# Optimization experiments

Hardware: AMD Instinct MI355X
Metric: run time of the kernel (lower is better)

The kernel has to match this reference:

```python
import jax, jax.numpy as jnp
import numpy as np


def setup_inputs() -> dict:
    key = jax.random.key(0)
    k1, k2, k3, k4 = jax.random.split(key, 4)
    N, F_in, F_out = 8192, 512, 256
    inp = jax.random.normal(k1, (N, F_in), dtype=jnp.float32)
    adj = jax.random.uniform(k2, (N, N), dtype=jnp.float32)
    stdv = 1.0 / np.sqrt(F_out)
    weight = jax.random.uniform(k3, (F_in, F_out), minval=-stdv, maxval=stdv, dtype=jnp.float32)
    b = jax.random.uniform(k4, (F_out,), minval=-stdv, maxval=stdv, dtype=jnp.float32)
    return {"input": inp, "adj": adj, "weight": weight, "b": b}


def reference(input, adj, weight, b):
    N = adj.shape[0]
    degree = jnp.sum(adj, axis=1)                      # [N]
    # A_tilde = 2*I - adj
    A_tilde = 2.0 * jnp.eye(N, dtype=adj.dtype) - adj
    d_inv_sqrt = 1.0 / jnp.sqrt(2.0 + degree)          # [N]
    # D^-1/2 @ A_tilde @ D^-1/2 as broadcasted row/col scaling (same math, O(N^2))
    L_sharpen = d_inv_sqrt[:, None] * A_tilde * d_inv_sqrt[None, :]
    support = input @ weight                           # [N, F_out]
    out = L_sharpen @ support + b                      # [N, F_out]
    return jax.nn.relu(out)
```

## Files before the change

kernel.cpp:

```cpp
#include <hip/hip_runtime.h>


typedef _Float16 h4 __attribute__((ext_vector_type(4)));
typedef _Float16 h8 __attribute__((ext_vector_type(8)));
typedef float f4 __attribute__((ext_vector_type(4)));

__device__ __forceinline__ void gload_lds16(const void* g, void* l) {
    __builtin_amdgcn_global_load_lds(
        (const __attribute__((address_space(1))) void*)g,
        (__attribute__((address_space(3))) void*)l, 16, 0, 0);
}

__global__ __launch_bounds__(256) void k0_wt(const float* __restrict__ weight,
                                             char* __restrict__ wt) {
    const int idx = blockIdx.x * 256 + threadIdx.x;
    const int k = idx >> 8, j = idx & 255;
    const _Float16 h = (_Float16)weight[idx];
    const int off = j * 1024 + ((k >> 6) << 7) + (((k & 63) << 1) ^ ((j & 7) << 4));
    *(_Float16*)(wt + off) = h;
}

__global__ __launch_bounds__(256) void k1_deg(const float* __restrict__ adj,
                                              float* __restrict__ dinv) {
    const int r = blockIdx.x;
    const float4* rp = (const float4*)(adj + (size_t)r * 8192);
    const int t = threadIdx.x;
    float s = 0.f;
#pragma unroll
    for (int i = 0; i < 8; ++i) {
        float4 v = rp[t + i * 256];
        s += (v.x + v.y) + (v.z + v.w);
    }
#pragma unroll
    for (int off = 32; off > 0; off >>= 1) s += __shfl_down(s, off, 64);
    __shared__ float part[4];
    if ((t & 63) == 0) part[t >> 6] = s;
    __syncthreads();
    if (t == 0) {
        float deg = (part[0] + part[1]) + (part[2] + part[3]);
        dinv[r] = 1.0f / sqrtf(2.0f + deg);
    }
}

__global__ __launch_bounds__(512) void k2_support(const float* __restrict__ input,
                                                  const char* __restrict__ wt,
                                                  const float* __restrict__ dinv,
                                                  char* __restrict__ sT) {
    __shared__ char smem[8192 + 32768];
    const int t = threadIdx.x, w = t >> 6, l = t & 63;
    const int r0 = (int)blockIdx.x * 64;
    const int ar = t >> 4, ac4 = t & 15;
    const int bj = l >> 3, bb = (l & 7) * 16;

    f4 acc[4][2] = {};

    for (int kt = 0; kt < 8; ++kt) {
        const int k0 = kt * 64;
        __syncthreads();
#pragma unroll
        for (int hh = 0; hh < 2; ++hh) {
            const int row = ar + hh * 32;
            float4 v = *(const float4*)(input + (size_t)(r0 + row) * 512 + k0 + ac4 * 4);
            h4 h;
            h[0] = (_Float16)v.x; h[1] = (_Float16)v.y;
            h[2] = (_Float16)v.z; h[3] = (_Float16)v.w;
            *(h4*)(smem + row * 128 + ((ac4 * 8) ^ ((row & 7) << 4))) = h;
        }
#pragma unroll
        for (int q = 0; q < 4; ++q) {
            const int c = w * 4 + q;
            gload_lds16(wt + (size_t)(c * 8 + bj) * 1024 + kt * 128 + bb,
                        smem + 8192 + c * 1024);
        }
        __syncthreads();
#pragma unroll
        for (int kk = 0; kk < 2; ++kk) {
            const int kb = (kk * 32 + ((l >> 4) << 3)) << 1;
            h8 b[2];
#pragma unroll
            for (int n = 0; n < 2; ++n) {
                const int j = w * 32 + n * 16 + (l & 15);
                b[n] = *(const h8*)(smem + 8192 + j * 128 + (kb ^ ((j & 7) << 4)));
            }
#pragma unroll
            for (int m = 0; m < 4; ++m) {
                const int r = m * 16 + (l & 15);
                h8 a = *(const h8*)(smem + r * 128 + (kb ^ ((r & 7) << 4)));
                acc[m][0] = __builtin_amdgcn_mfma_f32_16x16x32_f16(a, b[0], acc[m][0], 0, 0, 0);
                acc[m][1] = __builtin_amdgcn_mfma_f32_16x16x32_f16(a, b[1], acc[m][1], 0, 0, 0);
            }
        }
    }
#pragma unroll
    for (int m = 0; m < 4; ++m)
#pragma unroll
        for (int n = 0; n < 2; ++n) {
            const int j = w * 32 + n * 16 + (l & 15);
            const int k0r = r0 + m * 16 + ((l >> 4) << 2);
            h4 h;
#pragma unroll
            for (int r = 0; r < 4; ++r)
                h[r] = (_Float16)(dinv[k0r + r] * acc[m][n][r]);
            const int off = j * 16384 + ((k0r >> 6) << 7) +
                            (((k0r & 63) << 1) ^ ((j & 7) << 4));
            *(h4*)(sT + off) = h;
        }
}

__global__ __launch_bounds__(512, 4) void k3_spmm(const float* __restrict__ adj,
                                                  const char* __restrict__ sT,
                                                  float* __restrict__ part,
                                                  float* __restrict__ out,
                                                  int steps) {
    __shared__ __align__(16) char smem[2][40960];
    const int t = threadIdx.x;
    const int w = t >> 6, l = t & 63;
    const int wm = w >> 2, wn = w & 3;
    const int i0 = (int)blockIdx.x * 64;
    const int ks0 = (int)blockIdx.y * steps * 64;

    const int arow = t >> 3;
    const int ak8 = (t & 7) * 8;
    const int arow_g = i0 + arow;
    const float4* aptr = (const float4*)(adj + (size_t)arow_g * 8192 + ks0 + ak8);
    const int a_off = arow * 128 + (((t & 7) << 4) ^ ((arow & 7) << 4));

    const int bj = l >> 3, bb = (l & 7) * 16;
    const int chunk0 = ks0 >> 6;

    f4 acc[2][4] = {};

    auto stageB = [&](int kt, int buf) {
        char* bl = smem[buf] + 8192;
#pragma unroll
        for (int q = 0; q < 4; ++q) {
            const int c = w * 4 + q;
            gload_lds16(sT + (size_t)(c * 8 + bj) * 16384 + (chunk0 + kt) * 128 + bb,
                        bl + c * 1024);
        }
    };
    auto loadA = [&](int kt, float4& v0, float4& v1) {
        v0 = aptr[kt * 16];
        v1 = aptr[kt * 16 + 1];
    };
    auto writeA = [&](int kt, const float4 v0, const float4 v1, int buf) {
        const int kg = ks0 + kt * 64 + ak8;
        h8 h;
        const float* vv = (const float*)&v0;
#pragma unroll
        for (int e = 0; e < 4; ++e)
            h[e] = (_Float16)((arow_g == kg + e) ? 2.0f - vv[e] : -vv[e]);
        const float* vw = (const float*)&v1;
#pragma unroll
        for (int e = 0; e < 4; ++e)
            h[4 + e] = (_Float16)((arow_g == kg + 4 + e) ? 2.0f - vw[e] : -vw[e]);
        *(h8*)(smem[buf] + a_off) = h;
    };
    auto compute = [&](int buf) {
        const char* A = smem[buf];
        const char* B = smem[buf] + 8192;
#pragma unroll
        for (int kk = 0; kk < 2; ++kk) {
            const int ko = kk * 64 + ((l >> 4) << 4);
            h8 a[2], b[4];
#pragma unroll
            for (int m = 0; m < 2; ++m) {
                const int r = wm * 32 + m * 16 + (l & 15);
                a[m] = *(const h8*)(A + r * 128 + (ko ^ ((r & 7) << 4)));
            }
#pragma unroll
            for (int n = 0; n < 4; ++n) {
                const int j = wn * 64 + n * 16 + (l & 15);
                b[n] = *(const h8*)(B + j * 128 + (ko ^ ((j & 7) << 4)));
            }
#pragma unroll
            for (int m = 0; m < 2; ++m)
#pragma unroll
                for (int n = 0; n < 4; ++n)
                    acc[m][n] = __builtin_amdgcn_mfma_f32_16x16x32_f16(a[m], b[n], acc[m][n], 0, 0, 0);
        }
    };

    {
        float4 v0, v1;
        loadA(0, v0, v1);
        stageB(0, 0);
        writeA(0, v0, v1, 0);
        __syncthreads();
    }

    int cur = 0;
    for (int kt = 0; kt < steps; ++kt) {
        const bool pf = (kt + 1) < steps;
        float4 v0, v1;
        if (pf) {
            stageB(kt + 1, cur ^ 1);
            loadA(kt + 1, v0, v1);
        }
        compute(cur);
        if (pf) writeA(kt + 1, v0, v1, cur ^ 1);
        __syncthreads();
        cur ^= 1;
    }

    float* dst = (blockIdx.y == gridDim.y - 1) ? out
               : part + (size_t)blockIdx.y * (8192 * 256);
#pragma unroll
    for (int m = 0; m < 2; ++m)
#pragma unroll
        for (int n = 0; n < 4; ++n) {
            const int j = wn * 64 + n * 16 + (l & 15);
            const int ib = i0 + wm * 32 + m * 16 + ((l >> 4) << 2);
#pragma unroll
            for (int r = 0; r < 4; ++r)
                dst[(size_t)(ib + r) * 256 + j] = acc[m][n][r];
        }
}

__global__ __launch_bounds__(256) void k4_fin(const float* __restrict__ part,
                                              float* __restrict__ out,
                                              const float* __restrict__ dinv,
                                              const float* __restrict__ bias,
                                              int nsplit) {
    const int idx = blockIdx.x * 256 + threadIdx.x;
    float4 s = ((const float4*)out)[idx];
    for (int sp = 0; sp < nsplit - 1; ++sp)
        s += ((const float4*)(part + (size_t)sp * (8192 * 256)))[idx];
    const float dv = dinv[idx >> 6];
    const float4 b = ((const float4*)bias)[idx & 63];
    float4 r;
    r.x = fmaxf(dv * s.x + b.x, 0.f);
    r.y = fmaxf(dv * s.y + b.y, 0.f);
    r.z = fmaxf(dv * s.z + b.z, 0.f);
    r.w = fmaxf(dv * s.w + b.w, 0.f);
    ((float4*)out)[idx] = r;
}

extern "C" void kernel_launch(void* const* d_in, const int* in_sizes, int n_in,
                              void* d_out, int out_size, void* d_ws, size_t ws_size,
                              hipStream_t stream) {
    const float* input  = (const float*)d_in[0];
    const float* adj    = (const float*)d_in[1];
    const float* weight = (const float*)d_in[2];
    const float* bias   = (const float*)d_in[3];
    float* out = (float*)d_out;

    char* ws = (char*)d_ws;
    float* dinv = (float*)ws;
    char*  wt   = ws + 32768;
    char*  sT   = ws + 294912;
    float* part = (float*)(ws + 294912 + 4194304);

    const size_t base = 294912 + 4194304;
    int nsplit = 1;
    if (ws_size >= base + 3 * 8388608) nsplit = 4;
    else if (ws_size >= base + 1 * 8388608) nsplit = 2;
    const int steps = 128 / nsplit;

    k0_wt<<<512, 256, 0, stream>>>(weight, wt);
    k1_deg<<<8192, 256, 0, stream>>>(adj, dinv);
    k2_support<<<128, 512, 0, stream>>>(input, wt, dinv, sT);
    k3_spmm<<<dim3(128, nsplit), 512, 0, stream>>>(adj, sT, part, out, steps);
    k4_fin<<<2048, 256, 0, stream>>>(part, out, dinv, bias, nsplit);
}
```

Baseline: 143.2 us.

## Deepen adj prefetch in spmm with manual waitcnt pipelining; halve support tile

The spmm kernel now keeps adj loads two k-steps ahead using inline-asm global loads, explicit vmcnt waits and raw s_barrier, so the LDS writes of the next A tile overlap the MFMA compute of the current one. It also applies the identity-diagonal check only on the single k-tile that contains the diagonal. The support GEMM uses 32-row tiles across 256 blocks to put more workgroups on the device. The hand-written waitcnt counts rely on the exact number of outstanding loads, which is brittle. The extra in-flight registers may reduce occupancy.

Measured after the change: 137.7 us. 3.8% less time.

```diff
diff --git a/kernel.cpp b/kernel.cpp
--- a/kernel.cpp
+++ b/kernel.cpp
@@ -9,6 +9,14 @@
     __builtin_amdgcn_global_load_lds(
         (const __attribute__((address_space(1))) void*)g,
         (__attribute__((address_space(3))) void*)l, 16, 0, 0);
+}
+
+__device__ __forceinline__ void gload2(const float* p, f4& x, f4& y) {
+    asm volatile("global_load_dwordx4 %0, %2, off\n\t"
+                 "global_load_dwordx4 %1, %2, off offset:16"
+                 : "=&v"(x), "=&v"(y)
+                 : "v"(p)
+                 : "memory");
 }
 
 __global__ __launch_bounds__(256) void k0_wt(const float* __restrict__ weight,
@@ -46,61 +54,64 @@
                                                   const char* __restrict__ wt,
                                                   const float* __restrict__ dinv,
                                                   char* __restrict__ sT) {
-    __shared__ char smem[8192 + 32768];
+    __shared__ char smem[4096 + 32768];
     const int t = threadIdx.x, w = t >> 6, l = t & 63;
-    const int r0 = (int)blockIdx.x * 64;
-    const int ar = t >> 4, ac4 = t & 15;
+    const int r0 = (int)blockIdx.x * 32;
+    const int arow = t >> 4, ak4 = t & 15;
     const int bj = l >> 3, bb = (l & 7) * 16;
 
-    f4 acc[4][2] = {};
+    f4 acc[2][2] = {};
 
     for (int kt = 0; kt < 8; ++kt) {
         const int k0 = kt * 64;
         __syncthreads();
-#pragma unroll
-        for (int hh = 0; hh < 2; ++hh) {
-            const int row = ar + hh * 32;
-            float4 v = *(const float4*)(input + (size_t)(r0 + row) * 512 + k0 + ac4 * 4);
+        {
+            float4 v = *(const float4*)(input + (size_t)(r0 + arow) * 512 + k0 + ak4 * 4);
             h4 h;
             h[0] = (_Float16)v.x; h[1] = (_Float16)v.y;
             h[2] = (_Float16)v.z; h[3] = (_Float16)v.w;
-            *(h4*)(smem + row * 128 + ((ac4 * 8) ^ ((row & 7) << 4))) = h;
+            *(h4*)(smem + arow * 128 + ((ak4 * 8) ^ ((arow & 7) << 4)));
+            *(h4*)(smem + arow * 128 + ((ak4 * 8) ^ ((arow & 7) << 4))) = h;
         }
 #pragma unroll
         for (int q = 0; q < 4; ++q) {
-            const int c = w * 4 + q;
+            const int c = q * 8 + w;
             gload_lds16(wt + (size_t)(c * 8 + bj) * 1024 + kt * 128 + bb,
-                        smem + 8192 + c * 1024);
+                        smem + 4096 + c * 1024);
         }
         __syncthreads();
 #pragma unroll
         for (int kk = 0; kk < 2; ++kk) {
-            const int kb = (kk * 32 + ((l >> 4) << 3)) << 1;
-            h8 b[2];
+            const int ko = kk * 64 + ((l >> 4) << 4);
+            h8 a[2], b[2];
+#pragma unroll
+            for (int m = 0; m < 2; ++m) {
+                const int r = m * 16 + (l & 15);
+                a[m] = *(const h8*)(smem + r * 128 + (ko ^ ((r & 7) << 4)));
+            }
 #pragma unroll
             for (int n = 0; n < 2; ++n) {
                 const int j = w * 32 + n * 16 + (l & 15);
-                b[n] = *(const h8*)(smem + 8192 + j * 128 + (kb ^ ((j & 7) << 4)));
-            }
-#pragma unroll
-            for (int m = 0; m < 4; ++m) {
-                const int r = m * 16 + (l & 15);
-                h8 a = *(const h8*)(smem + r * 128 + (kb ^ ((r & 7) << 4)));
-                acc[m][0] = __builtin_amdgcn_mfma_f32_16x16x32_f16(a, b[0], acc[m][0], 0, 0, 0);
-                acc[m][1] = __builtin_amdgcn_mfma_f32_16x16x32_f16(a, b[1], acc[m][1], 0, 0, 0);
-            }
-        }
-    }
-#pragma unroll
-    for (int m = 0; m < 4; ++m)
+                b[n] = *(const h8*)(smem + 4096 + j * 128 + (ko ^ ((j & 7) << 4)));
+            }
+#pragma unroll
+            for (int m = 0; m < 2; ++m)
+#pragma unroll
+                for (int n = 0; n < 2; ++n)
+                    acc[m][n] = __builtin_amdgcn_mfma_f32_16x16x32_f16(a[m], b[n], acc[m][n], 0, 0, 0);
+        }
+    }
+#pragma unroll
+    for (int m = 0; m < 2; ++m)
 #pragma unroll
         for (int n = 0; n < 2; ++n) {
             const int j = w * 32 + n * 16 + (l & 15);
             const int k0r = r0 + m * 16 + ((l >> 4) << 2);
             h4 h;
 #pragma unroll
-            for (int r = 0; r < 4; ++r)
-                h[r] = (_Float16)(dinv[k0r + r] * acc[m][n][r]);
+            for (int r = 0; r < 2; ++r) h[r] = (_Float16)(dinv[k0r + r] * acc[m][n][r]);
+#pragma unroll
+            for (int r = 2; r < 4; ++r) h[r] = (_Float16)(dinv[k0r + r] * acc[m][n][r]);
             const int off = j * 16384 + ((k0r >> 6) << 7) +
                             (((k0r & 63) << 1) ^ ((j & 7) << 4));
             *(h4*)(sT + off) = h;
@@ -118,11 +129,12 @@
     const int wm = w >> 2, wn = w & 3;
     const int i0 = (int)blockIdx.x * 64;
     const int ks0 = (int)blockIdx.y * steps * 64;
+    const int dkt = (i0 - ks0) >> 6;
 
     const int arow = t >> 3;
     const int ak8 = (t & 7) * 8;
     const int arow_g = i0 + arow;
-    const float4* aptr = (const float4*)(adj + (size_t)arow_g * 8192 + ks0 + ak8);
+    const float* aptr = adj + (size_t)arow_g * 8192 + ks0 + ak8;
     const int a_off = arow * 128 + (((t & 7) << 4) ^ ((arow & 7) << 4));
 
     const int bj = l >> 3, bb = (l & 7) * 16;
@@ -130,8 +142,8 @@
 
     f4 acc[2][4] = {};
 
-    auto stageB = [&](int kt, int buf) {
-        char* bl = smem[buf] + 8192;
+    auto stageB = [&](int kt, char* buf) {
+        char* bl = buf + 8192;
 #pragma unroll
         for (int q = 0; q < 4; ++q) {
             const int c = w * 4 + q;
@@ -139,26 +151,27 @@
                         bl + c * 1024);
         }
     };
-    auto loadA = [&](int kt, float4& v0, float4& v1) {
-        v0 = aptr[kt * 16];
-        v1 = aptr[kt * 16 + 1];
-    };
-    auto writeA = [&](int kt, const float4 v0, const float4 v1, int buf) {
+    auto writeA = [&](char* buf, int kt, const f4 x, const f4 y) {
         const int kg = ks0 + kt * 64 + ak8;
         h8 h;
-        const float* vv = (const float*)&v0;
-#pragma unroll
-        for (int e = 0; e < 4; ++e)
-            h[e] = (_Float16)((arow_g == kg + e) ? 2.0f - vv[e] : -vv[e]);
-        const float* vw = (const float*)&v1;
-#pragma unroll
-        for (int e = 0; e < 4; ++e)
-            h[4 + e] = (_Float16)((arow_g == kg + 4 + e) ? 2.0f - vw[e] : -vw[e]);
-        *(h8*)(smem[buf] + a_off) = h;
-    };
-    auto compute = [&](int buf) {
-        const char* A = smem[buf];
-        const char* B = smem[buf] + 8192;
+        if (kt == dkt) {
+#pragma unroll
+            for (int e = 0; e < 4; ++e)
+                h[e] = (_Float16)((arow_g == kg + e) ? 2.0f - x[e] : -x[e]);
+#pragma unroll
+            for (int e = 0; e < 4; ++e)
+                h[4 + e] = (_Float16)((arow_g == kg + 4 + e) ? 2.0f - y[e] : -y[e]);
+        } else {
+#pragma unroll
+            for (int e = 0; e < 4; ++e) h[e] = (_Float16)(-x[e]);
+#pragma unroll
+            for (int e = 0; e < 4; ++e) h[4 + e] = (_Float16)(-y[e]);
+        }
+        *(h8*)(buf + a_off) = h;
+    };
+    auto compute = [&](const char* buf) {
+        const char* A = buf;
+        const char* B = buf + 8192;
 #pragma unroll
         for (int kk = 0; kk < 2; ++kk) {
             const int ko = kk * 64 + ((l >> 4) << 4);
@@ -181,26 +194,41 @@
         }
     };
 
+    f4 fx0, fy0, fx1, fy1;
+
+    gload2(aptr, fx0, fy0);
+    gload2(aptr + 64, fx1, fy1);
+    stageB(0, smem[0]);
+    asm volatile("s_waitcnt vmcnt(6)" : "+v"(fx0), "+v"(fy0) :: "memory");
+    __builtin_amdgcn_sched_barrier(0);
+    writeA(smem[0], 0, fx0, fy0);
+    asm volatile("s_waitcnt vmcnt(2) lgkmcnt(0)\n\ts_barrier" ::: "memory");
+    __builtin_amdgcn_sched_barrier(0);
+
+    auto body = [&](int kt, f4& xc, f4& yc, f4& xn, f4& yn, char* bufC, char* bufN) {
+        stageB(kt + 1, bufN);
+        gload2(aptr + (size_t)(kt + 2) * 64, xc, yc);
+        asm volatile("s_waitcnt vmcnt(6)" : "+v"(xn), "+v"(yn) :: "memory");
+        __builtin_amdgcn_sched_barrier(0);
+        writeA(bufN, kt + 1, xn, yn);
+        compute(bufC);
+        asm volatile("s_waitcnt vmcnt(2) lgkmcnt(0)\n\ts_barrier" ::: "memory");
+        __builtin_amdgcn_sched_barrier(0);
+    };
+
+    for (int kt2 = 0; kt2 + 2 < steps; kt2 += 2) {
+        body(kt2,     fx0, fy0, fx1, fy1, smem[0], smem[1]);
+        body(kt2 + 1, fx1, fy1, fx0, fy0, smem[1], smem[0]);
+    }
     {
-        float4 v0, v1;
-        loadA(0, v0, v1);
-        stageB(0, 0);
-        writeA(0, v0, v1, 0);
-        __syncthreads();
-    }
-
-    int cur = 0;
-    for (int kt = 0; kt < steps; ++kt) {
-        const bool pf = (kt + 1) < steps;
-        float4 v0, v1;
-        if (pf) {
-            stageB(kt + 1, cur ^ 1);
-            loadA(kt + 1, v0, v1);
-        }
-        compute(cur);
-        if (pf) writeA(kt + 1, v0, v1, cur ^ 1);
-        __syncthreads();
-        cur ^= 1;
+        stageB(steps - 1, smem[1]);
+        asm volatile("s_waitcnt vmcnt(4)" : "+v"(fx1), "+v"(fy1) :: "memory");
+        __builtin_amdgcn_sched_barrier(0);
+        writeA(smem[1], steps - 1, fx1, fy1);
+        compute(smem[0]);
+        asm volatile("s_waitcnt vmcnt(0) lgkmcnt(0)\n\ts_barrier" ::: "memory");
+        __builtin_amdgcn_sched_barrier(0);
+        compute(smem[1]);
     }
 
     float* dst = (blockIdx.y == gridDim.y - 1) ? out
@@ -259,7 +287,7 @@
 
     k0_wt<<<512, 256, 0, stream>>>(weight, wt);
     k1_deg<<<8192, 256, 0, stream>>>(adj, dinv);
-    k2_support<<<128, 512, 0, stream>>>(input, wt, dinv, sT);
+    k2_support<<<256, 512, 0, stream>>>(input, wt, dinv, sT);
     k3_spmm<<<dim3(128, nsplit), 512, 0, stream>>>(adj, sT, part, out, steps);
     k4_fin<<<2048, 256, 0, stream>>>(part, out, dinv, bias, nsplit);
 }
```
